# Kernel optimization log

Measured on AMD Instinct MI355X. Metric: run time of the kernel, lower is better.

Reference implementation:

```python
import jax, jax.numpy as jnp
import numpy as np

WIDTH = 2048
NUM_HEADS = 16
HEAD_DIM = WIDTH // NUM_HEADS  # 128
ROPE_DIMS = HEAD_DIM // 2      # 64, partial rotary
WINDOW = 512
ROPE_BASE = 10000.0
NEG_INF = -1e9


def apply_rope(x, dims, offset=0, base=ROPE_BASE):
    # x: [B, H, L, hd]; non-traditional (half-split) rotary on first `dims` dims.
    L = x.shape[2]
    half = dims // 2
    pos = (offset + jnp.arange(L)).astype(x.dtype)                     # [L]
    inv_freq = jnp.exp(-jnp.log(jnp.asarray(base, x.dtype)) * (jnp.arange(0, dims, 2).astype(x.dtype) / dims))  # [half]
    theta = pos[:, None] * inv_freq[None, :]                           # [L, half]
    cos = jnp.cos(theta)[None, None]                                   # [1,1,L,half]
    sin = jnp.sin(theta)[None, None]
    x1 = x[..., :half]
    x2 = x[..., half:dims]
    rest = x[..., dims:]
    rx1 = x1 * cos - x2 * sin
    rx2 = x1 * sin + x2 * cos
    return jnp.concatenate([rx1, rx2, rest], axis=-1)


def setup_inputs() -> dict:
    key = jax.random.key(0)
    ks = jax.random.split(key, 6)
    B, L, D, hd = 2, 2048, WIDTH, HEAD_DIM
    x = jax.random.normal(ks[0], (B, L, D), dtype=jnp.float32)
    Wq = jax.random.normal(ks[1], (D, D), dtype=jnp.float32) * 0.02
    Wk = jax.random.normal(ks[2], (D, hd), dtype=jnp.float32) * 0.02
    Wv = jax.random.normal(ks[3], (D, hd), dtype=jnp.float32) * 0.02
    Wo = jax.random.normal(ks[4], (D, D), dtype=jnp.float32) * 0.02
    bo = jax.random.normal(ks[5], (D,), dtype=jnp.float32) * 0.02
    return {"x": x, "Wq": Wq, "Wk": Wk, "Wv": Wv, "Wo": Wo, "bo": bo}


def reference(x, Wq, Wk, Wv, Wo, bo):
    B, L, D = x.shape
    H, hd = NUM_HEADS, HEAD_DIM
    scale = hd ** (-0.5)

    q = (x @ Wq).reshape(B, L, H, hd).transpose(0, 2, 1, 3)   # [B,H,L,hd]
    k = (x @ Wk).reshape(B, L, 1, hd).transpose(0, 2, 1, 3)   # [B,1,L,hd] (MQA)
    v = (x @ Wv).reshape(B, L, 1, hd).transpose(0, 2, 1, 3)

    q = apply_rope(q, ROPE_DIMS)
    k = apply_rope(k, ROPE_DIMS)

    # sliding-window causal mask: attend iff 0 <= i - j < WINDOW
    i = jnp.arange(L)[:, None]
    j = jnp.arange(L)[None, :]
    allowed = (i - j >= 0) & (i - j < WINDOW)                  # [L,L]
    mask = jnp.where(allowed, 0.0, NEG_INF).astype(x.dtype)

    scores = jnp.einsum("bhqd,bkd->bhqk", q, k[:, 0]) * scale  # [B,H,L,L]
    scores = scores + mask[None, None]
    attn = jax.nn.softmax(scores, axis=-1)
    out = jnp.einsum("bhqk,bkd->bhqd", attn, v[:, 0])          # [B,H,L,hd]
    out = out.transpose(0, 2, 1, 3).reshape(B, L, D)
    return out @ Wo + bo
```

## Files before the change

kernel.cpp:

```cpp
#include <hip/hip_runtime.h>
#include <hip/hip_bf16.h>
#include <stdint.h>


typedef float  f32x4  __attribute__((ext_vector_type(4)));
typedef __bf16 bf16x8 __attribute__((ext_vector_type(8)));

#define ASYNC_LD16(gp, lp)                                                     \
  __builtin_amdgcn_global_load_lds(                                            \
      (__attribute__((address_space(1))) void*)(gp),                           \
      (__attribute__((address_space(3))) void*)(lp), 16, 0, 0)

__global__ void cvt_bf16(const float* __restrict__ in,
                         __hip_bfloat16* __restrict__ out, int n4) {
  const int i = blockIdx.x * 256 + threadIdx.x;
  if (i >= n4) return;
  const float4 v = ((const float4*)in)[i];
  __align__(8) __hip_bfloat16 t[4] = {
      __float2bfloat16(v.x), __float2bfloat16(v.y),
      __float2bfloat16(v.z), __float2bfloat16(v.w)};
  *(uint2*)(out + (size_t)i * 4) = *(uint2*)t;
}

__global__ void transpose_cvt(const float* __restrict__ in,
                              __hip_bfloat16* __restrict__ out, int R, int C) {
  __shared__ float t[32][33];
  const int c0 = blockIdx.x * 32;
  const int r0 = blockIdx.y * 32;
  const int x = threadIdx.x, y = threadIdx.y;
#pragma unroll
  for (int i = 0; i < 32; i += 8)
    t[y + i][x] = in[(size_t)(r0 + y + i) * C + c0 + x];
  __syncthreads();
#pragma unroll
  for (int i = 0; i < 32; i += 8)
    out[(size_t)(c0 + y + i) * R + r0 + x] = __float2bfloat16(t[x][y + i]);
}

__global__ void vt_cvt(const __hip_bfloat16* __restrict__ src,
                       __hip_bfloat16* __restrict__ dst) {
  __shared__ __hip_bfloat16 t[32][33];
  const int c0 = blockIdx.x * 32;
  const int r0 = blockIdx.y * 32;
  const int x = threadIdx.x, y = threadIdx.y;
#pragma unroll
  for (int i = 0; i < 32; i += 8)
    t[y + i][x] = src[(size_t)(r0 + y + i) * 128 + c0 + x];
  __syncthreads();
  const int bb = r0 >> 11;
  const int l0 = r0 & 2047;
#pragma unroll
  for (int i = 0; i < 32; i += 8)
    dst[((size_t)(bb * 128 + c0 + y + i)) * 2048 + l0 + x] = t[x][y + i];
}

__device__ __forceinline__ void gemm_core(const __bf16* __restrict__ A,
                                          const __bf16* __restrict__ BT,
                                          int K, __bf16* As, __bf16* Bs,
                                          f32x4 (&acc)[4][4]) {
  const int tid = threadIdx.x;
  const int wave = tid >> 6;
  const int lane = tid & 63;
  const int m0 = blockIdx.y * 128;
  const int n0 = blockIdx.x * 128;
  const int wm = (wave & 1) * 64;
  const int wn = (wave >> 1) * 64;
  const int lrow = lane & 15;
  const int quad = lane >> 4;
  const int rdoff = ((quad ^ ((lrow >> 1) & 3)) * 8);

  const int idx0 = wave * 128 + lane;
  const int idx1 = idx0 + 64;
  const int ar0 = idx0 >> 2, ar1 = idx1 >> 2;
  const int ac0 = (((idx0 & 3) ^ ((ar0 >> 1) & 3)) * 8);
  const int ac1 = (((idx1 & 3) ^ ((ar1 >> 1) & 3)) * 8);

  for (int k0 = 0; k0 < K; k0 += 32) {
    ASYNC_LD16(A + (size_t)(m0 + ar0) * K + k0 + ac0, As + (wave * 2 + 0) * 512);
    ASYNC_LD16(A + (size_t)(m0 + ar1) * K + k0 + ac1, As + (wave * 2 + 1) * 512);
    ASYNC_LD16(BT + (size_t)(n0 + ar0) * K + k0 + ac0, Bs + (wave * 2 + 0) * 512);
    ASYNC_LD16(BT + (size_t)(n0 + ar1) * K + k0 + ac1, Bs + (wave * 2 + 1) * 512);
    __syncthreads();
    bf16x8 af[4], bf[4];
#pragma unroll
    for (int i = 0; i < 4; i++)
      af[i] = *(const bf16x8*)&As[(wm + i * 16 + lrow) * 32 + rdoff];
#pragma unroll
    for (int j = 0; j < 4; j++)
      bf[j] = *(const bf16x8*)&Bs[(wn + j * 16 + lrow) * 32 + rdoff];
#pragma unroll
    for (int i = 0; i < 4; i++)
#pragma unroll
      for (int j = 0; j < 4; j++)
        acc[i][j] = __builtin_amdgcn_mfma_f32_16x16x32_bf16(af[i], bf[j],
                                                            acc[i][j], 0, 0, 0);
    __syncthreads();
  }
}

__global__ __launch_bounds__(256) void gemm_qkv(
    const __bf16* __restrict__ A, const __bf16* __restrict__ BT,
    __hip_bfloat16* __restrict__ qd, __hip_bfloat16* __restrict__ kd,
    __hip_bfloat16* __restrict__ vd, int K) {
  __shared__ __align__(16) __bf16 As[128 * 32];
  __shared__ __align__(16) __bf16 Bs[128 * 32];
  f32x4 acc[4][4];
  const f32x4 zero = {0.f, 0.f, 0.f, 0.f};
#pragma unroll
  for (int i = 0; i < 4; i++)
#pragma unroll
    for (int j = 0; j < 4; j++) acc[i][j] = zero;
  gemm_core(A, BT, K, As, Bs, acc);

  const int tid = threadIdx.x;
  const int wave = tid >> 6;
  const int lane = tid & 63;
  const int quad = lane >> 4;
  const int ln = lane & 15;
  const int m0 = blockIdx.y * 128;
  const int n0 = blockIdx.x * 128;
  const int wm = (wave & 1) * 64;
  const int wn = (wave >> 1) * 64;

  __hip_bfloat16* dst;
  int dstride, dcol;
  if (n0 < 2048) {
    dst = qd; dstride = 2048; dcol = n0;
  } else if (n0 == 2048) {
    dst = kd; dstride = 128; dcol = 0;
  } else {
    dst = vd; dstride = 128; dcol = 0;
  }
  const bool dorope = (wn == 0) && (n0 <= 2048);
  float invf0 = 0.f, invf1 = 0.f;
  if (dorope) {
    invf0 = expf(-0.28782313662425574f * (float)ln);
    invf1 = expf(-0.28782313662425574f * (float)(16 + ln));
  }

#pragma unroll
  for (int i = 0; i < 4; i++) {
#pragma unroll
    for (int r = 0; r < 4; r++) {
      const int row = m0 + wm + i * 16 + quad * 4 + r;
      float o0 = acc[i][0][r], o1 = acc[i][1][r];
      float o2 = acc[i][2][r], o3 = acc[i][3][r];
      if (dorope) {
        const float pos = (float)(row & 2047);
        float s0, c0, s1, c1;
        __sincosf(pos * invf0, &s0, &c0);
        __sincosf(pos * invf1, &s1, &c1);
        const float a0 = o0, b0 = o2, a1 = o1, b1 = o3;
        o0 = a0 * c0 - b0 * s0;
        o2 = a0 * s0 + b0 * c0;
        o1 = a1 * c1 - b1 * s1;
        o3 = a1 * s1 + b1 * c1;
      }
      __hip_bfloat16* rp = dst + (size_t)row * dstride + dcol + wn + ln;
      rp[0]  = __float2bfloat16(o0);
      rp[16] = __float2bfloat16(o1);
      rp[32] = __float2bfloat16(o2);
      rp[48] = __float2bfloat16(o3);
    }
  }
}

__global__ __launch_bounds__(256) void gemm_out(
    const __bf16* __restrict__ A, const __bf16* __restrict__ BT,
    float* __restrict__ C, const float* __restrict__ bias, int N, int K) {
  __shared__ __align__(16) __bf16 As[128 * 32];
  __shared__ __align__(16) __bf16 Bs[128 * 32];
  f32x4 acc[4][4];
  const f32x4 zero = {0.f, 0.f, 0.f, 0.f};
#pragma unroll
  for (int i = 0; i < 4; i++)
#pragma unroll
    for (int j = 0; j < 4; j++) acc[i][j] = zero;
  gemm_core(A, BT, K, As, Bs, acc);

  const int tid = threadIdx.x;
  const int wave = tid >> 6;
  const int lane = tid & 63;
  const int m0 = blockIdx.y * 128;
  const int n0 = blockIdx.x * 128;
  const int wm = (wave & 1) * 64;
  const int wn = (wave >> 1) * 64;
  const int lrow = lane & 15;
#pragma unroll
  for (int j = 0; j < 4; j++) {
    const int col = n0 + wn + j * 16 + lrow;
    const float bv = bias[col];
#pragma unroll
    for (int i = 0; i < 4; i++) {
#pragma unroll
      for (int r = 0; r < 4; r++) {
        const int row = m0 + wm + i * 16 + (lane >> 4) * 4 + r;
        C[(size_t)row * N + col] = acc[i][j][r] + bv;
      }
    }
  }
}

__global__ __launch_bounds__(256) void attn_mfma(
    const __bf16* __restrict__ qb,
    const __bf16* __restrict__ kb,
    const __bf16* __restrict__ vtb,
    __hip_bfloat16* __restrict__ o)
{
  __shared__ __align__(16) __bf16 Ks[4][64 * 32];
  __shared__ __align__(16) __bf16 Vs[2][128 * 32];
  __shared__ __align__(16) __bf16 Ps[4][2][16 * 32];
  const int tid = threadIdx.x;
  const int wave = tid >> 6;
  const int lane = tid & 63;
  const int quad = lane >> 4;
  const int ln = lane & 15;
  const int bid = blockIdx.x;
  const int q0 = (bid & 31) * 64;
  const int h = (bid >> 5) & 15;
  const int b = bid >> 9;

  const __bf16* qrow =
      qb + ((size_t)(b * 2048 + q0 + wave * 16 + ln)) * 2048 + h * 128;
  bf16x8 qf[4];
#pragma unroll
  for (int ks = 0; ks < 4; ks++)
    qf[ks] = *(const bf16x8*)(qrow + ks * 32 + quad * 8);

  f32x4 oacc[8];
  const f32x4 zero = {0.f, 0.f, 0.f, 0.f};
#pragma unroll
  for (int nb = 0; nb < 8; nb++) oacc[nb] = zero;
  float li[4] = {0.f, 0.f, 0.f, 0.f};
  const float scale = 0.08838834764831845f;

  const __bf16* kbase = kb + (size_t)b * 2048 * 128;
  const __bf16* vbase = vtb + (size_t)b * 128 * 2048;

  const int tstart = (q0 >= 512) ? 0 : (512 - q0) / 64;
  for (int t = tstart; t < 9; ++t) {
    const int jt = q0 - 512 + 64 * t;
    __syncthreads();
    {
      const int key4 = lane >> 2, uu = lane & 3;
#pragma unroll
      for (int i = 0; i < 4; ++i) {
        const int c = wave * 4 + i;
        const int ks = c & 3, keybase = (c >> 2) * 16;
        ASYNC_LD16(kbase + (size_t)(jt + keybase + key4) * 128 + ks * 32 + uu * 8,
                   &Ks[ks][keybase * 32]);
      }
#pragma unroll
      for (int i = 0; i < 4; ++i) {
        const int c = wave * 4 + i;
        const int p = c & 1, dbase = (c >> 1) * 16;
        ASYNC_LD16(vbase + (size_t)(dbase + key4) * 2048 + jt + p * 32 + uu * 8,
                   &Vs[p][dbase * 32]);
      }
    }
    __syncthreads();

    f32x4 sacc[4];
#pragma unroll
    for (int j = 0; j < 4; j++) sacc[j] = zero;
#pragma unroll
    for (int j = 0; j < 4; j++)
#pragma unroll
      for (int ks = 0; ks < 4; ks++) {
        const bf16x8 kf = *(const bf16x8*)&Ks[ks][(j * 16 + ln) * 32 + quad * 8];
        sacc[j] = __builtin_amdgcn_mfma_f32_16x16x32_bf16(qf[ks], kf, sacc[j],
                                                          0, 0, 0);
      }

#pragma unroll
    for (int j = 0; j < 4; j++)
#pragma unroll
      for (int r = 0; r < 4; r++) {
        float v = sacc[j][r] * scale;
        const int rowidx = wave * 16 + quad * 4 + r;
        const int colidx = j * 16 + ln;
        if (t == 0) v = (rowidx < colidx) ? v : -1e30f;
        if (t == 8) v = (rowidx >= colidx) ? v : -1e30f;
        v = fminf(v, 60.f);
        const float p = __expf(v);
        li[r] += p;
        Ps[wave][j >> 1][(quad * 4 + r) * 32 + (j & 1) * 16 + ln] = (__bf16)p;
      }

    const bf16x8 pf0 = *(const bf16x8*)&Ps[wave][0][ln * 32 + quad * 8];
    const bf16x8 pf1 = *(const bf16x8*)&Ps[wave][1][ln * 32 + quad * 8];
#pragma unroll
    for (int nb = 0; nb < 8; nb++) {
      const bf16x8 vf0 = *(const bf16x8*)&Vs[0][(nb * 16 + ln) * 32 + quad * 8];
      const bf16x8 vf1 = *(const bf16x8*)&Vs[1][(nb * 16 + ln) * 32 + quad * 8];
      oacc[nb] =
          __builtin_amdgcn_mfma_f32_16x16x32_bf16(pf0, vf0, oacc[nb], 0, 0, 0);
      oacc[nb] =
          __builtin_amdgcn_mfma_f32_16x16x32_bf16(pf1, vf1, oacc[nb], 0, 0, 0);
    }
  }

#pragma unroll
  for (int off = 1; off < 16; off <<= 1)
#pragma unroll
    for (int r = 0; r < 4; r++) li[r] += __shfl_xor(li[r], off);

  __hip_bfloat16* obase =
      o + ((size_t)(b * 2048 + q0 + wave * 16 + quad * 4)) * 2048 + h * 128 + ln;
#pragma unroll
  for (int r = 0; r < 4; r++) {
    const float inv = 1.0f / li[r];
#pragma unroll
    for (int nb = 0; nb < 8; nb++)
      obase[(size_t)r * 2048 + nb * 16] = __float2bfloat16(oacc[nb][r] * inv);
  }
}

extern "C" void kernel_launch(void* const* d_in, const int* in_sizes, int n_in,
                              void* d_out, int out_size, void* d_ws,
                              size_t ws_size, hipStream_t stream) {
  const float* x = (const float*)d_in[0];
  const float* Wq = (const float*)d_in[1];
  const float* Wk = (const float*)d_in[2];
  const float* Wv = (const float*)d_in[3];
  const float* Wo = (const float*)d_in[4];
  const float* bo = (const float*)d_in[5];
  float* out = (float*)d_out;

  char* w = (char*)d_ws;
  auto alloc = [&](size_t bytes) {
    void* p = (void*)w;
    w += (bytes + 255) & ~(size_t)255;
    return p;
  };
  __bf16* xb = (__bf16*)alloc(4096ull * 2048 * 2);
  __hip_bfloat16* wqkvT = (__hip_bfloat16*)alloc(2304ull * 2048 * 2);
  __hip_bfloat16* woT = (__hip_bfloat16*)alloc(2048ull * 2048 * 2);
  __hip_bfloat16* qbuf = (__hip_bfloat16*)alloc(4096ull * 2048 * 2);
  __hip_bfloat16* kbuf = (__hip_bfloat16*)alloc(4096ull * 128 * 2);
  __hip_bfloat16* vbuf = (__hip_bfloat16*)alloc(4096ull * 128 * 2);
  __hip_bfloat16* vtb = (__hip_bfloat16*)alloc(4096ull * 128 * 2);
  __hip_bfloat16* attnb = (__hip_bfloat16*)xb;

  cvt_bf16<<<8192, 256, 0, stream>>>(x, (__hip_bfloat16*)xb, 2097152);
  transpose_cvt<<<dim3(64, 64), dim3(32, 8), 0, stream>>>(Wq, wqkvT, 2048, 2048);
  transpose_cvt<<<dim3(4, 64), dim3(32, 8), 0, stream>>>(
      Wk, wqkvT + 2048ull * 2048, 2048, 128);
  transpose_cvt<<<dim3(4, 64), dim3(32, 8), 0, stream>>>(
      Wv, wqkvT + 2176ull * 2048, 2048, 128);
  transpose_cvt<<<dim3(64, 64), dim3(32, 8), 0, stream>>>(Wo, woT, 2048, 2048);

  gemm_qkv<<<dim3(18, 32), 256, 0, stream>>>(xb, (const __bf16*)wqkvT, qbuf,
                                             kbuf, vbuf, 2048);

  vt_cvt<<<dim3(4, 128), dim3(32, 8), 0, stream>>>(vbuf, vtb);

  attn_mfma<<<1024, 256, 0, stream>>>((const __bf16*)qbuf, (const __bf16*)kbuf,
                                      (const __bf16*)vtb, attnb);

  gemm_out<<<dim3(16, 32), 256, 0, stream>>>((const __bf16*)attnb,
                                             (const __bf16*)woT, out, bo, 2048,
                                             2048);
}
```

Measured before the change: 279.9 us.

## Merge weight transposes, fuse V transpose into QKV GEMM, deepen K tile, widen attention tile

Four weight transpose launches become one combined kernel. The V transpose now happens in the QKV GEMM epilogue, which removes the vt_cvt pass and the vbuf round trip. The GEMM core stages 64 K-elements per sync instead of 32, halving barrier count at the cost of doubled LDS. The attention kernel has each wave handle two 16-row query groups, so K/V tiles are reused across 128 queries per block and the block count halves, at the cost of more registers and fewer blocks.

```diff
diff --git a/kernel.cpp b/kernel.cpp
--- a/kernel.cpp
+++ b/kernel.cpp
@@ -22,42 +22,42 @@
   *(uint2*)(out + (size_t)i * 4) = *(uint2*)t;
 }
 
-__global__ void transpose_cvt(const float* __restrict__ in,
-                              __hip_bfloat16* __restrict__ out, int R, int C) {
+__global__ __launch_bounds__(256) void transpose_all(
+    const float* __restrict__ Wq, const float* __restrict__ Wk,
+    const float* __restrict__ Wv, const float* __restrict__ Wo,
+    __hip_bfloat16* __restrict__ wqkvT, __hip_bfloat16* __restrict__ woT) {
   __shared__ float t[32][33];
-  const int c0 = blockIdx.x * 32;
-  const int r0 = blockIdx.y * 32;
-  const int x = threadIdx.x, y = threadIdx.y;
+  const int bid = blockIdx.x;
+  const float* src;
+  __hip_bfloat16* dst;
+  int C, cb, rb;
+  if (bid < 4096) {
+    src = Wq; dst = wqkvT; C = 2048; cb = bid & 63; rb = bid >> 6;
+  } else if (bid < 4352) {
+    const int l = bid - 4096;
+    src = Wk; dst = wqkvT + 2048ull * 2048; C = 128; cb = l & 3; rb = l >> 2;
+  } else if (bid < 4608) {
+    const int l = bid - 4352;
+    src = Wv; dst = wqkvT + 2176ull * 2048; C = 128; cb = l & 3; rb = l >> 2;
+  } else {
+    const int l = bid - 4608;
+    src = Wo; dst = woT; C = 2048; cb = l & 63; rb = l >> 6;
+  }
+  const int c0 = cb * 32, r0 = rb * 32;
+  const int x = threadIdx.x & 31, y = threadIdx.x >> 5;
 #pragma unroll
   for (int i = 0; i < 32; i += 8)
-    t[y + i][x] = in[(size_t)(r0 + y + i) * C + c0 + x];
+    t[y + i][x] = src[(size_t)(r0 + y + i) * C + c0 + x];
   __syncthreads();
 #pragma unroll
   for (int i = 0; i < 32; i += 8)
-    out[(size_t)(c0 + y + i) * R + r0 + x] = __float2bfloat16(t[x][y + i]);
-}
-
-__global__ void vt_cvt(const __hip_bfloat16* __restrict__ src,
-                       __hip_bfloat16* __restrict__ dst) {
-  __shared__ __hip_bfloat16 t[32][33];
-  const int c0 = blockIdx.x * 32;
-  const int r0 = blockIdx.y * 32;
-  const int x = threadIdx.x, y = threadIdx.y;
-#pragma unroll
-  for (int i = 0; i < 32; i += 8)
-    t[y + i][x] = src[(size_t)(r0 + y + i) * 128 + c0 + x];
-  __syncthreads();
-  const int bb = r0 >> 11;
-  const int l0 = r0 & 2047;
-#pragma unroll
-  for (int i = 0; i < 32; i += 8)
-    dst[((size_t)(bb * 128 + c0 + y + i)) * 2048 + l0 + x] = t[x][y + i];
-}
-
-__device__ __forceinline__ void gemm_core(const __bf16* __restrict__ A,
-                                          const __bf16* __restrict__ BT,
-                                          int K, __bf16* As, __bf16* Bs,
-                                          f32x4 (&acc)[4][4]) {
+    dst[(size_t)(c0 + y + i) * 2048 + r0 + x] = __float2bfloat16(t[x][y + i]);
+}
+
+__device__ __forceinline__ void gemm_core64(const __bf16* __restrict__ A,
+                                            const __bf16* __restrict__ BT,
+                                            int K, __bf16* As, __bf16* Bs,
+                                            f32x4 (&acc)[4][4]) {
   const int tid = threadIdx.x;
   const int wave = tid >> 6;
   const int lane = tid & 63;
@@ -65,35 +65,53 @@
   const int n0 = blockIdx.x * 128;
   const int wm = (wave & 1) * 64;
   const int wn = (wave >> 1) * 64;
-  const int lrow = lane & 15;
+  const int ln = lane & 15;
   const int quad = lane >> 4;
-  const int rdoff = ((quad ^ ((lrow >> 1) & 3)) * 8);
-
-  const int idx0 = wave * 128 + lane;
-  const int idx1 = idx0 + 64;
-  const int ar0 = idx0 >> 2, ar1 = idx1 >> 2;
-  const int ac0 = (((idx0 & 3) ^ ((ar0 >> 1) & 3)) * 8);
-  const int ac1 = (((idx1 & 3) ^ ((ar1 >> 1) & 3)) * 8);
-
-  for (int k0 = 0; k0 < K; k0 += 32) {
-    ASYNC_LD16(A + (size_t)(m0 + ar0) * K + k0 + ac0, As + (wave * 2 + 0) * 512);
-    ASYNC_LD16(A + (size_t)(m0 + ar1) * K + k0 + ac1, As + (wave * 2 + 1) * 512);
-    ASYNC_LD16(BT + (size_t)(n0 + ar0) * K + k0 + ac0, Bs + (wave * 2 + 0) * 512);
-    ASYNC_LD16(BT + (size_t)(n0 + ar1) * K + k0 + ac1, Bs + (wave * 2 + 1) * 512);
+  const int rdoff = (quad ^ ((ln >> 1) & 3)) * 8;
+
+  size_t goff[4];
+  int ldsoff[4];
+#pragma unroll
+  for (int i = 0; i < 4; i++) {
+    const int cidx = (wave * 4 + i) * 64 + lane;
+    const int p = cidx >> 9;
+    const int pidx = cidx & 511;
+    const int row = pidx >> 2;
+    const int cc = pidx & 3;
+    const int cg = cc ^ ((row >> 1) & 3);
+    goff[i] = (size_t)row * K + p * 32 + cg * 8;
+    ldsoff[i] = (wave * 4 + i) * 512;
+  }
+  const __bf16* Abase = A + (size_t)m0 * K;
+  const __bf16* Bbase = BT + (size_t)n0 * K;
+
+  for (int k0 = 0; k0 < K; k0 += 64) {
+#pragma unroll
+    for (int i = 0; i < 4; i++)
+      ASYNC_LD16(Abase + k0 + goff[i], As + ldsoff[i]);
+#pragma unroll
+    for (int i = 0; i < 4; i++)
+      ASYNC_LD16(Bbase + k0 + goff[i], Bs + ldsoff[i]);
     __syncthreads();
-    bf16x8 af[4], bf[4];
+    bf16x8 af[4][2], bf[4][2];
 #pragma unroll
     for (int i = 0; i < 4; i++)
-      af[i] = *(const bf16x8*)&As[(wm + i * 16 + lrow) * 32 + rdoff];
+#pragma unroll
+      for (int p = 0; p < 2; p++)
+        af[i][p] = *(const bf16x8*)&As[p * 4096 + (wm + i * 16 + ln) * 32 + rdoff];
 #pragma unroll
     for (int j = 0; j < 4; j++)
-      bf[j] = *(const bf16x8*)&Bs[(wn + j * 16 + lrow) * 32 + rdoff];
-#pragma unroll
-    for (int i = 0; i < 4; i++)
-#pragma unroll
-      for (int j = 0; j < 4; j++)
-        acc[i][j] = __builtin_amdgcn_mfma_f32_16x16x32_bf16(af[i], bf[j],
-                                                            acc[i][j], 0, 0, 0);
+#pragma unroll
+      for (int p = 0; p < 2; p++)
+        bf[j][p] = *(const bf16x8*)&Bs[p * 4096 + (wn + j * 16 + ln) * 32 + rdoff];
+#pragma unroll
+    for (int p = 0; p < 2; p++)
+#pragma unroll
+      for (int i = 0; i < 4; i++)
+#pragma unroll
+        for (int j = 0; j < 4; j++)
+          acc[i][j] = __builtin_amdgcn_mfma_f32_16x16x32_bf16(af[i][p], bf[j][p],
+                                                              acc[i][j], 0, 0, 0);
     __syncthreads();
   }
 }
@@ -101,16 +119,16 @@
 __global__ __launch_bounds__(256) void gemm_qkv(
     const __bf16* __restrict__ A, const __bf16* __restrict__ BT,
     __hip_bfloat16* __restrict__ qd, __hip_bfloat16* __restrict__ kd,
-    __hip_bfloat16* __restrict__ vd, int K) {
-  __shared__ __align__(16) __bf16 As[128 * 32];
-  __shared__ __align__(16) __bf16 Bs[128 * 32];
+    __hip_bfloat16* __restrict__ vtd, int K) {
+  __shared__ __align__(16) __bf16 As[128 * 64];
+  __shared__ __align__(16) __bf16 Bs[128 * 64];
   f32x4 acc[4][4];
   const f32x4 zero = {0.f, 0.f, 0.f, 0.f};
 #pragma unroll
   for (int i = 0; i < 4; i++)
 #pragma unroll
     for (int j = 0; j < 4; j++) acc[i][j] = zero;
-  gemm_core(A, BT, K, As, Bs, acc);
+  gemm_core64(A, BT, K, As, Bs, acc);
 
   const int tid = threadIdx.x;
   const int wave = tid >> 6;
@@ -122,16 +140,32 @@
   const int wm = (wave & 1) * 64;
   const int wn = (wave >> 1) * 64;
 
+  if (n0 == 2176) {
+    const int bb = m0 >> 11;
+    const int mloc = m0 & 2047;
+#pragma unroll
+    for (int i = 0; i < 4; i++) {
+      const int rb = mloc + wm + i * 16 + quad * 4;
+#pragma unroll
+      for (int j = 0; j < 4; j++) {
+        const int col = wn + j * 16 + ln;
+        __align__(8) __hip_bfloat16 t4[4];
+#pragma unroll
+        for (int r = 0; r < 4; r++) t4[r] = __float2bfloat16(acc[i][j][r]);
+        *(uint2*)(vtd + ((size_t)(bb * 128 + col)) * 2048 + rb) = *(uint2*)t4;
+      }
+    }
+    return;
+  }
+
   __hip_bfloat16* dst;
   int dstride, dcol;
   if (n0 < 2048) {
     dst = qd; dstride = 2048; dcol = n0;
-  } else if (n0 == 2048) {
+  } else {
     dst = kd; dstride = 128; dcol = 0;
-  } else {
-    dst = vd; dstride = 128; dcol = 0;
-  }
-  const bool dorope = (wn == 0) && (n0 <= 2048);
+  }
+  const bool dorope = (wn == 0);
   float invf0 = 0.f, invf1 = 0.f;
   if (dorope) {
     invf0 = expf(-0.28782313662425574f * (float)ln);
@@ -168,15 +202,15 @@
 __global__ __launch_bounds__(256) void gemm_out(
     const __bf16* __restrict__ A, const __bf16* __restrict__ BT,
     float* __restrict__ C, const float* __restrict__ bias, int N, int K) {
-  __shared__ __align__(16) __bf16 As[128 * 32];
-  __shared__ __align__(16) __bf16 Bs[128 * 32];
+  __shared__ __align__(16) __bf16 As[128 * 64];
+  __shared__ __align__(16) __bf16 Bs[128 * 64];
   f32x4 acc[4][4];
   const f32x4 zero = {0.f, 0.f, 0.f, 0.f};
 #pragma unroll
   for (int i = 0; i < 4; i++)
 #pragma unroll
     for (int j = 0; j < 4; j++) acc[i][j] = zero;
-  gemm_core(A, BT, K, As, Bs, acc);
+  gemm_core64(A, BT, K, As, Bs, acc);
 
   const int tid = threadIdx.x;
   const int wave = tid >> 6;
@@ -209,36 +243,41 @@
 {
   __shared__ __align__(16) __bf16 Ks[4][64 * 32];
   __shared__ __align__(16) __bf16 Vs[2][128 * 32];
-  __shared__ __align__(16) __bf16 Ps[4][2][16 * 32];
+  __shared__ __align__(16) __bf16 Ps[4][2][2][512];
   const int tid = threadIdx.x;
   const int wave = tid >> 6;
   const int lane = tid & 63;
   const int quad = lane >> 4;
   const int ln = lane & 15;
   const int bid = blockIdx.x;
-  const int q0 = (bid & 31) * 64;
-  const int h = (bid >> 5) & 15;
-  const int b = bid >> 9;
-
-  const __bf16* qrow =
-      qb + ((size_t)(b * 2048 + q0 + wave * 16 + ln)) * 2048 + h * 128;
-  bf16x8 qf[4];
-#pragma unroll
-  for (int ks = 0; ks < 4; ks++)
-    qf[ks] = *(const bf16x8*)(qrow + ks * 32 + quad * 8);
-
-  f32x4 oacc[8];
+  const int q0 = (bid & 15) * 128;
+  const int h = (bid >> 4) & 15;
+  const int b = bid >> 8;
+
+  bf16x8 qf[2][4];
+#pragma unroll
+  for (int g = 0; g < 2; g++) {
+    const __bf16* qrow =
+        qb + ((size_t)(b * 2048 + q0 + wave * 32 + g * 16 + ln)) * 2048 + h * 128;
+#pragma unroll
+    for (int ks = 0; ks < 4; ks++)
+      qf[g][ks] = *(const bf16x8*)(qrow + ks * 32 + quad * 8);
+  }
+
+  f32x4 oacc[2][8];
   const f32x4 zero = {0.f, 0.f, 0.f, 0.f};
 #pragma unroll
-  for (int nb = 0; nb < 8; nb++) oacc[nb] = zero;
-  float li[4] = {0.f, 0.f, 0.f, 0.f};
+  for (int g = 0; g < 2; g++)
+#pragma unroll
+    for (int nb = 0; nb < 8; nb++) oacc[g][nb] = zero;
+  float li[2][4] = {{0.f, 0.f, 0.f, 0.f}, {0.f, 0.f, 0.f, 0.f}};
   const float scale = 0.08838834764831845f;
 
   const __bf16* kbase = kb + (size_t)b * 2048 * 128;
   const __bf16* vbase = vtb + (size_t)b * 128 * 2048;
 
   const int tstart = (q0 >= 512) ? 0 : (512 - q0) / 64;
-  for (int t = tstart; t < 9; ++t) {
+  for (int t = tstart; t < 10; ++t) {
     const int jt = q0 - 512 + 64 * t;
     __syncthreads();
     {
@@ -260,59 +299,76 @@
     }
     __syncthreads();
 
-    f32x4 sacc[4];
-#pragma unroll
-    for (int j = 0; j < 4; j++) sacc[j] = zero;
+    f32x4 sacc[2][4];
+#pragma unroll
+    for (int g = 0; g < 2; g++)
+#pragma unroll
+      for (int j = 0; j < 4; j++) sacc[g][j] = zero;
 #pragma unroll
     for (int j = 0; j < 4; j++)
 #pragma unroll
       for (int ks = 0; ks < 4; ks++) {
         const bf16x8 kf = *(const bf16x8*)&Ks[ks][(j * 16 + ln) * 32 + quad * 8];
-        sacc[j] = __builtin_amdgcn_mfma_f32_16x16x32_bf16(qf[ks], kf, sacc[j],
-                                                          0, 0, 0);
-      }
-
-#pragma unroll
-    for (int j = 0; j < 4; j++)
-#pragma unroll
-      for (int r = 0; r < 4; r++) {
-        float v = sacc[j][r] * scale;
-        const int rowidx = wave * 16 + quad * 4 + r;
-        const int colidx = j * 16 + ln;
-        if (t == 0) v = (rowidx < colidx) ? v : -1e30f;
-        if (t == 8) v = (rowidx >= colidx) ? v : -1e30f;
-        v = fminf(v, 60.f);
-        const float p = __expf(v);
-        li[r] += p;
-        Ps[wave][j >> 1][(quad * 4 + r) * 32 + (j & 1) * 16 + ln] = (__bf16)p;
-      }
-
-    const bf16x8 pf0 = *(const bf16x8*)&Ps[wave][0][ln * 32 + quad * 8];
-    const bf16x8 pf1 = *(const bf16x8*)&Ps[wave][1][ln * 32 + quad * 8];
+#pragma unroll
+        for (int g = 0; g < 2; g++)
+          sacc[g][j] = __builtin_amdgcn_mfma_f32_16x16x32_bf16(qf[g][ks], kf,
+                                                               sacc[g][j], 0, 0, 0);
+      }
+
+#pragma unroll
+    for (int g = 0; g < 2; g++)
+#pragma unroll
+      for (int j = 0; j < 4; j++)
+#pragma unroll
+        for (int r = 0; r < 4; r++) {
+          float v = sacc[g][j][r] * scale;
+          const int d0 = (wave * 32 + g * 16 + quad * 4 + r) - (j * 16 + ln);
+          if (t <= 1 && d0 >= (t << 6)) v = -1e30f;
+          if (t >= 8 && d0 < ((t - 8) << 6)) v = -1e30f;
+          v = fminf(v, 60.f);
+          const float p = __expf(v);
+          li[g][r] += p;
+          Ps[wave][g][j >> 1][(quad * 4 + r) * 32 + (j & 1) * 16 + ln] = (__bf16)p;
+        }
+
+    const bf16x8 pf00 = *(const bf16x8*)&Ps[wave][0][0][ln * 32 + quad * 8];
+    const bf16x8 pf01 = *(const bf16x8*)&Ps[wave][0][1][ln * 32 + quad * 8];
+    const bf16x8 pf10 = *(const bf16x8*)&Ps[wave][1][0][ln * 32 + quad * 8];
+    const bf16x8 pf11 = *(const bf16x8*)&Ps[wave][1][1][ln * 32 + quad * 8];
 #pragma unroll
     for (int nb = 0; nb < 8; nb++) {
       const bf16x8 vf0 = *(const bf16x8*)&Vs[0][(nb * 16 + ln) * 32 + quad * 8];
       const bf16x8 vf1 = *(const bf16x8*)&Vs[1][(nb * 16 + ln) * 32 + quad * 8];
-      oacc[nb] =
-          __builtin_amdgcn_mfma_f32_16x16x32_bf16(pf0, vf0, oacc[nb], 0, 0, 0);
-      oacc[nb] =
-          __builtin_amdgcn_mfma_f32_16x16x32_bf16(pf1, vf1, oacc[nb], 0, 0, 0);
+      oacc[0][nb] =
+          __builtin_amdgcn_mfma_f32_16x16x32_bf16(pf00, vf0, oacc[0][nb], 0, 0, 0);
+      oacc[0][nb] =
+          __builtin_amdgcn_mfma_f32_16x16x32_bf16(pf01, vf1, oacc[0][nb], 0, 0, 0);
+      oacc[1][nb] =
+          __builtin_amdgcn_mfma_f32_16x16x32_bf16(pf10, vf0, oacc[1][nb], 0, 0, 0);
+      oacc[1][nb] =
+          __builtin_amdgcn_mfma_f32_16x16x32_bf16(pf11, vf1, oacc[1][nb], 0, 0, 0);
     }
   }
 
 #pragma unroll
   for (int off = 1; off < 16; off <<= 1)
 #pragma unroll
-    for (int r = 0; r < 4; r++) li[r] += __shfl_xor(li[r], off);
-
-  __hip_bfloat16* obase =
-      o + ((size_t)(b * 2048 + q0 + wave * 16 + quad * 4)) * 2048 + h * 128 + ln;
-#pragma unroll
-  for (int r = 0; r < 4; r++) {
-    const float inv = 1.0f / li[r];
-#pragma unroll
-    for (int nb = 0; nb < 8; nb++)
-      obase[(size_t)r * 2048 + nb * 16] = __float2bfloat16(oacc[nb][r] * inv);
+    for (int g = 0; g < 2; g++)
+#pragma unroll
+      for (int r = 0; r < 4; r++) li[g][r] += __shfl_xor(li[g][r], off);
+
+#pragma unroll
+  for (int g = 0; g < 2; g++) {
+    __hip_bfloat16* obase =
+        o + ((size_t)(b * 2048 + q0 + wave * 32 + g * 16 + quad * 4)) * 2048 +
+        h * 128 + ln;
+#pragma unroll
+    for (int r = 0; r < 4; r++) {
+      const float inv = 1.0f / li[g][r];
+#pragma unroll
+      for (int nb = 0; nb < 8; nb++)
+        obase[(size_t)r * 2048 + nb * 16] = __float2bfloat16(oacc[g][nb][r] * inv);
+    }
   }
 }
 
@@ -338,25 +394,17 @@
   __hip_bfloat16* woT = (__hip_bfloat16*)alloc(2048ull * 2048 * 2);
   __hip_bfloat16* qbuf = (__hip_bfloat16*)alloc(4096ull * 2048 * 2);
   __hip_bfloat16* kbuf = (__hip_bfloat16*)alloc(4096ull * 128 * 2);
-  __hip_bfloat16* vbuf = (__hip_bfloat16*)alloc(4096ull * 128 * 2);
   __hip_bfloat16* vtb = (__hip_bfloat16*)alloc(4096ull * 128 * 2);
   __hip_bfloat16* attnb = (__hip_bfloat16*)xb;
 
   cvt_bf16<<<8192, 256, 0, stream>>>(x, (__hip_bfloat16*)xb, 2097152);
-  transpose_cvt<<<dim3(64, 64), dim3(32, 8), 0, stream>>>(Wq, wqkvT, 2048, 2048);
-  transpose_cvt<<<dim3(4, 64), dim3(32, 8), 0, stream>>>(
-      Wk, wqkvT + 2048ull * 2048, 2048, 128);
-  transpose_cvt<<<dim3(4, 64), dim3(32, 8), 0, stream>>>(
-      Wv, wqkvT + 2176ull * 2048, 2048, 128);
-  transpose_cvt<<<dim3(64, 64), dim3(32, 8), 0, stream>>>(Wo, woT, 2048, 2048);
+  transpose_all<<<8704, 256, 0, stream>>>(Wq, Wk, Wv, Wo, wqkvT, woT);
 
   gemm_qkv<<<dim3(18, 32), 256, 0, stream>>>(xb, (const __bf16*)wqkvT, qbuf,
-                                             kbuf, vbuf, 2048);
-
-  vt_cvt<<<dim3(4, 128), dim3(32, 8), 0, stream>>>(vbuf, vtb);
-
-  attn_mfma<<<1024, 256, 0, stream>>>((const __bf16*)qbuf, (const __bf16*)kbuf,
-                                      (const __bf16*)vtb, attnb);
+                                             kbuf, vtb, 2048);
+
+  attn_mfma<<<512, 256, 0, stream>>>((const __bf16*)qbuf, (const __bf16*)kbuf,
+                                     (const __bf16*)vtb, attnb);
 
   gemm_out<<<dim3(16, 32), 256, 0, stream>>>((const __bf16*)attnb,
                                              (const __bf16*)woT, out, bo, 2048,
```

Measured after the change: 269.2 us. 1.04x faster.
